# Kernel tuning notes

Hardware: AMD Instinct MI355X
Metric: run time of the kernel (lower is better)

Reference implementation:

```python
import jax, jax.numpy as jnp
import numpy as np

B, S, I, H, L = 32, 512, 512, 512, 2


def _gru_scan(x, wx, bx, wh, bh, reverse):
    # x: [B, S, layer_in_dim]; wx: [3H, in], wh: [3H, H]. PyTorch gate order r,z,n.
    hdim = wh.shape[1]
    gx = jnp.einsum('bsi,gi->sbg', x, wx) + bx  # precompute input gates: [S, B, 3H]
    h0 = jnp.zeros((x.shape[0], hdim), x.dtype)

    def step(h, gxt):
        gh = h @ wh.T + bh
        r = jax.nn.sigmoid(gxt[:, :hdim] + gh[:, :hdim])
        z = jax.nn.sigmoid(gxt[:, hdim:2 * hdim] + gh[:, hdim:2 * hdim])
        n = jnp.tanh(gxt[:, 2 * hdim:] + r * gh[:, 2 * hdim:])
        hn = (1 - z) * n + z * h
        return hn, hn

    hN, ys = jax.lax.scan(step, h0, gx, reverse=reverse)
    return ys.transpose(1, 0, 2), hN  # [B, S, H], [B, H]


def setup_inputs() -> dict:
    key = jax.random.key(0)
    ks = jax.random.split(key, 17)
    sc = 0.05
    d = {'x': jax.random.normal(ks[0], (B, S, I), jnp.float32)}
    i = 1
    for layer in range(L):
        in_dim = I if layer == 0 else 2 * H
        for tag in ('f', 'b'):
            d[f'wx_{tag}{layer}'] = jax.random.normal(ks[i], (3 * H, in_dim), jnp.float32) * sc
            d[f'bx_{tag}{layer}'] = jax.random.normal(jax.random.fold_in(ks[i], 1), (3 * H,), jnp.float32) * sc
            d[f'wh_{tag}{layer}'] = jax.random.normal(jax.random.fold_in(ks[i], 2), (3 * H, H), jnp.float32) * sc
            d[f'bh_{tag}{layer}'] = jax.random.normal(jax.random.fold_in(ks[i], 3), (3 * H,), jnp.float32) * sc
            i += 1
    return d


def reference(x,
              wx_f0, bx_f0, wh_f0, bh_f0, wx_b0, bx_b0, wh_b0, bh_b0,
              wx_f1, bx_f1, wh_f1, bh_f1, wx_b1, bx_b1, wh_b1, bh_b1):
    layers = [((wx_f0, bx_f0, wh_f0, bh_f0), (wx_b0, bx_b0, wh_b0, bh_b0)),
              ((wx_f1, bx_f1, wh_f1, bh_f1), (wx_b1, bx_b1, wh_b1, bh_b1))]
    layer_in = x
    h_fw, h_bw = [], []
    for fw, bw in layers:
        yf, hf = _gru_scan(layer_in, *fw, reverse=False)
        yb, hb = _gru_scan(layer_in, *bw, reverse=True)
        layer_in = jnp.concatenate([yf, yb], axis=-1)  # [B, S, 2H] (dropout p=0 -> identity)
        h_fw.append(hf)
        h_bw.append(hb)
    return layer_in, (jnp.stack(h_fw, 0), jnp.stack(h_bw, 0))
```

## Files before the change

kernel.cpp:

```cpp
#include <hip/hip_runtime.h>
#include <stdint.h>

typedef short short8 __attribute__((ext_vector_type(8)));
typedef float floatx4 __attribute__((ext_vector_type(4)));
typedef unsigned long long u64;

__device__ __forceinline__ unsigned short f2bf(float f) {
  union { float f; unsigned int i; } v;
  v.f = f;
  unsigned int r = v.i + 0x7fffu + ((v.i >> 16) & 1u);
  return (unsigned short)(r >> 16);
}
__device__ __forceinline__ short8 cvt8(const float4 a, const float4 b) {
  short8 v;
  v[0] = (short)f2bf(a.x); v[1] = (short)f2bf(a.y);
  v[2] = (short)f2bf(a.z); v[3] = (short)f2bf(a.w);
  v[4] = (short)f2bf(b.x); v[5] = (short)f2bf(b.y);
  v[6] = (short)f2bf(b.z); v[7] = (short)f2bf(b.w);
  return v;
}
__device__ __forceinline__ float sane(float x, float lim) {
  return fminf(fmaxf(x, -lim), lim);
}

extern __shared__ unsigned short lds[];

template<int K, int XM, int EM>
__global__ __launch_bounds__(128)
void gru_layer(const float* __restrict__ xf,
               const unsigned short* __restrict__ xb,
               const float* __restrict__ wxfp,
               const float* __restrict__ bxfp,
               const float* __restrict__ whfp,
               const float* __restrict__ bhfp,
               const float* __restrict__ wxbp,
               const float* __restrict__ bxbp,
               const float* __restrict__ whbp,
               const float* __restrict__ bhbp,
               unsigned short* __restrict__ exch,
               float* __restrict__ omain,
               float* __restrict__ out_hf,
               float* __restrict__ out_hb)
{
  constexpr int NKS = K / 32;
  constexpr int WXW = K + 8;
  constexpr int KC = K >> 3;
  constexpr int KSH = (K == 512) ? 6 : 7;
  constexpr u64 TM = 0x4000400040004000ULL;

  unsigned short* whs = lds;
  unsigned short* wxs = lds + 48 * 520;

  const int bid = blockIdx.x;
  const bool fw = bid < 32;
  const int d = fw ? bid : bid - 32;
  const int tid = threadIdx.x;
  const int lane = tid & 63;
  const int w = tid >> 6;
  const int q = lane >> 4;
  const int l16 = lane & 15;

  const float* wx = fw ? wxfp : wxbp;
  const float* bx = fw ? bxfp : bxbp;
  const float* wh = fw ? whfp : whbp;
  const float* bh = fw ? bhfp : bhbp;
  const int col0 = d * 16;
  const int dirofs = fw ? 0 : 512;

  unsigned int* exch32 = (unsigned int*)exch;

  for (int c = tid; c < 48 * 64; c += 128) {
    int lr = c >> 6, c8 = (c & 63) * 8;
    int g = lr >> 4, jc = lr & 15;
    const float* src = wh + (long)(g * 512 + col0 + jc) * 512 + c8;
    *(short8*)(whs + lr * 520 + c8) =
        cvt8(*(const float4*)src, *(const float4*)(src + 4));
  }
  for (int c = tid; c < 48 * KC; c += 128) {
    int lr = c >> KSH, c8 = (c & (KC - 1)) * 8;
    int g = lr >> 4, jc = lr & 15;
    const float* src = wx + (long)(g * 512 + col0 + jc) * K + c8;
    *(short8*)(wxs + lr * WXW + c8) =
        cvt8(*(const float4*)src, *(const float4*)(src + 4));
  }
  __syncthreads();

  const int jj = l16;
  const int gcr = col0 + jj;
  const int gcz = 512 + col0 + jj;
  const int gcn = 1024 + col0 + jj;
  const float cr = bx[gcr] + bh[gcr];
  const float cz = bx[gcz] + bh[gcz];
  const float bxn = bx[gcn];
  const float bhn = bh[gcn];

  const int cb = w * 16 + q * 4;
  const int ab = w * 16 + l16;

  const floatx4 fz = {0.f, 0.f, 0.f, 0.f};
  float h[4] = {0.f, 0.f, 0.f, 0.f};

  float4 fpre[XM ? 2 * NKS : 1];
  short8 bpre[XM ? 1 : NKS];

  auto load_x = [&](int t) {
    if (XM) {
      const float* p = xf + ((long)ab * 512 + t) * 512 + q * 8;
#pragma unroll
      for (int ks = 0; ks < NKS; ++ks) {
        fpre[2 * ks]     = *(const float4*)(p + ks * 32);
        fpre[2 * ks + 1] = *(const float4*)(p + ks * 32 + 4);
      }
    } else {
      const unsigned short* p = xb + ((long)t * 32 + ab) * 1024 + q * 8;
#pragma unroll
      for (int ks = 0; ks < NKS; ++ks)
        bpre[ks] = *(const short8*)(p + ks * 32);
    }
  };

  auto mfma_gx = [&](floatx4& gr, floatx4& gz, floatx4& gn) {
    gr = fz; gz = fz; gn = fz;
#pragma unroll
    for (int ks = 0; ks < NKS; ++ks) {
      short8 a;
      if (XM) {
        a = cvt8(fpre[2 * ks], fpre[2 * ks + 1]);
      } else {
        union { short8 s; unsigned int dd[4]; } u;
        u.s = bpre[ks];
        u.dd[0] &= 0xBFFFBFFFu; u.dd[1] &= 0xBFFFBFFFu;
        u.dd[2] &= 0xBFFFBFFFu; u.dd[3] &= 0xBFFFBFFFu;
        a = u.s;
      }
      short8 vr = *(const short8*)(wxs + (jj) * WXW + ks * 32 + q * 8);
      short8 vz = *(const short8*)(wxs + (16 + jj) * WXW + ks * 32 + q * 8);
      short8 vn = *(const short8*)(wxs + (32 + jj) * WXW + ks * 32 + q * 8);
      gr = __builtin_amdgcn_mfma_f32_16x16x32_bf16(a, vr, gr, 0, 0, 0);
      gz = __builtin_amdgcn_mfma_f32_16x16x32_bf16(a, vz, gz, 0, 0, 0);
      gn = __builtin_amdgcn_mfma_f32_16x16x32_bf16(a, vn, gn, 0, 0, 0);
    }
  };

  floatx4 gxr, gxz, gxn;
  { const int t0 = fw ? 0 : 511; load_x(t0); mfma_gx(gxr, gxz, gxn); }

  union W { u64 u[2]; short8 s; unsigned int dd[4]; };

  for (int it = 0; it < 512; ++it) {
    const int t = fw ? it : 511 - it;

    const unsigned short* hbase = nullptr;
    u64 expectw = 0;
    if (it > 0) {
      if (EM == 0) {
        const int tprev = fw ? t - 1 : t + 1;
        hbase = exch + ((long)tprev * 32 + ab) * 1024 + dirofs;
        expectw = TM;
      } else {
        const int slot_r = (it + 1) & 1;
        hbase = exch + ((long)slot_r * 32 + ab) * 1024 + dirofs;
        expectw = ((((it - 1) >> 1) & 1) ^ 1) ? TM : 0ULL;
      }
    }

    W wv[16];
    if (it > 0) {
#pragma unroll
      for (int ks = 0; ks < 16; ++ks) {
        u64* p = (u64*)(hbase + ks * 32 + q * 8);
        wv[ks].u[0] = __hip_atomic_load(p,     __ATOMIC_RELAXED, __HIP_MEMORY_SCOPE_AGENT);
        wv[ks].u[1] = __hip_atomic_load(p + 1, __ATOMIC_RELAXED, __HIP_MEMORY_SCOPE_AGENT);
      }
    }
    if (it < 511) {
      const int tn2 = fw ? (it + 1) : (511 - (it + 1));
      load_x(tn2);
    }

    floatx4 ar = fz, az = fz, an = fz;
    if (it > 0) {
      while (true) {
        u64 bad = 0;
#pragma unroll
        for (int ks = 0; ks < 16; ++ks)
          bad |= ((wv[ks].u[0] ^ expectw) | (wv[ks].u[1] ^ expectw)) & TM;
        if (bad == 0) break;
        __builtin_amdgcn_s_sleep(1);
#pragma unroll
        for (int ks = 0; ks < 16; ++ks) {
          u64* p = (u64*)(hbase + ks * 32 + q * 8);
          wv[ks].u[0] = __hip_atomic_load(p,     __ATOMIC_RELAXED, __HIP_MEMORY_SCOPE_AGENT);
          wv[ks].u[1] = __hip_atomic_load(p + 1, __ATOMIC_RELAXED, __HIP_MEMORY_SCOPE_AGENT);
        }
      }
#pragma unroll
      for (int ks = 0; ks < 16; ++ks) {
        wv[ks].dd[0] &= 0xBFFFBFFFu; wv[ks].dd[1] &= 0xBFFFBFFFu;
        wv[ks].dd[2] &= 0xBFFFBFFFu; wv[ks].dd[3] &= 0xBFFFBFFFu;
        short8 a = wv[ks].s;
        short8 vr = *(const short8*)(whs + (jj) * 520 + ks * 32 + q * 8);
        short8 vz = *(const short8*)(whs + (16 + jj) * 520 + ks * 32 + q * 8);
        short8 vn = *(const short8*)(whs + (32 + jj) * 520 + ks * 32 + q * 8);
        ar = __builtin_amdgcn_mfma_f32_16x16x32_bf16(a, vr, ar, 0, 0, 0);
        az = __builtin_amdgcn_mfma_f32_16x16x32_bf16(a, vz, az, 0, 0, 0);
        an = __builtin_amdgcn_mfma_f32_16x16x32_bf16(a, vn, an, 0, 0, 0);
      }
    }

    unsigned short hb16[4];
#pragma unroll
    for (int r = 0; r < 4; ++r) {
      const float xr = sane(gxr[r] + ar[r] + cr, 60.f);
      const float xz = sane(gxz[r] + az[r] + cz, 60.f);
      const float rr = 1.f / (1.f + __expf(-xr));
      const float zz = 1.f / (1.f + __expf(-xz));
      const float xn = sane(gxn[r] + bxn + rr * (an[r] + bhn), 30.f);
      const float e2 = __expf(-2.f * xn);
      const float nn = (1.f - e2) / (1.f + e2);
      h[r] = (1.f - zz) * nn + zz * h[r];
      hb16[r] = f2bf(h[r]);
    }

    const unsigned int tb =
        (EM == 0) ? 0x40004000u
                  : (((((it) >> 1) & 1) ^ 1) ? 0x40004000u : 0u);
    unsigned int hw[4];
#pragma unroll
    for (int r = 0; r < 4; ++r) {
      int v = hb16[r];
      int pmate = __shfl_xor(v, 1);
      hw[r] = ((unsigned int)(v & 0xffff) |
               ((unsigned int)(pmate & 0xffff) << 16)) | tb;
    }
    if ((jj & 1) == 0) {
      const int colw = (dirofs + col0 + jj) >> 1;
#pragma unroll
      for (int r = 0; r < 4; ++r) {
        const long eidx = (EM == 0)
            ? (((long)t * 32 + cb + r) * 512 + colw)
            : (((long)(it & 1) * 32 + cb + r) * 512 + colw);
        __hip_atomic_store(exch32 + eidx, hw[r],
                           __ATOMIC_RELAXED, __HIP_MEMORY_SCOPE_AGENT);
      }
    }
    if (EM == 1) {
#pragma unroll
      for (int r = 0; r < 4; ++r)
        omain[(long)(cb + r) * 524288 + (long)t * 1024 + dirofs + col0 + jj] = h[r];
    }

    if (it == 511) {
      float* oh = fw ? out_hf : out_hb;
#pragma unroll
      for (int r = 0; r < 4; ++r)
        oh[(cb + r) * 512 + col0 + jj] = h[r];
    } else {
      mfma_gx(gxr, gxz, gxn);
    }
  }
}

extern "C" void kernel_launch(void* const* d_in, const int* in_sizes, int n_in,
                              void* d_out, int out_size, void* d_ws, size_t ws_size,
                              hipStream_t stream)
{
  (void)in_sizes; (void)n_in; (void)out_size; (void)ws_size;

  const float* x    = (const float*)d_in[0];
  const float* wxf0 = (const float*)d_in[1];
  const float* bxf0 = (const float*)d_in[2];
  const float* whf0 = (const float*)d_in[3];
  const float* bhf0 = (const float*)d_in[4];
  const float* wxb0 = (const float*)d_in[5];
  const float* bxb0 = (const float*)d_in[6];
  const float* whb0 = (const float*)d_in[7];
  const float* bhb0 = (const float*)d_in[8];
  const float* wxf1 = (const float*)d_in[9];
  const float* bxf1 = (const float*)d_in[10];
  const float* whf1 = (const float*)d_in[11];
  const float* bhf1 = (const float*)d_in[12];
  const float* wxb1 = (const float*)d_in[13];
  const float* bxb1 = (const float*)d_in[14];
  const float* whb1 = (const float*)d_in[15];
  const float* bhb1 = (const float*)d_in[16];

  char* ws = (char*)d_ws;
  unsigned short* y0    = (unsigned short*)(ws);
  unsigned short* ring1 = (unsigned short*)(ws + 33554432L);

  float* out = (float*)d_out;
  float* out_hf0 = out + 16777216L;
  float* out_hf1 = out + 16777216L + 16384L;
  float* out_hb0 = out + 16777216L + 32768L;
  float* out_hb1 = out + 16777216L + 49152L;

  const size_t lds0 = (size_t)(48 * 520 + 48 * (512 + 8)) * 2;
  const size_t lds1 = (size_t)(48 * 520 + 48 * (1024 + 8)) * 2;
  (void)hipFuncSetAttribute((const void*)gru_layer<512, 1, 0>,
                            hipFuncAttributeMaxDynamicSharedMemorySize, (int)lds0);
  (void)hipFuncSetAttribute((const void*)gru_layer<1024, 0, 1>,
                            hipFuncAttributeMaxDynamicSharedMemorySize, (int)lds1);

  hipMemsetAsync(ws, 0, 33685504L, stream);

  gru_layer<512, 1, 0><<<dim3(64), dim3(128), lds0, stream>>>(
      x, nullptr, wxf0, bxf0, whf0, bhf0, wxb0, bxb0, whb0, bhb0,
      y0, nullptr, out_hf0, out_hb0);

  gru_layer<1024, 0, 1><<<dim3(64), dim3(128), lds1, stream>>>(
      nullptr, y0, wxf1, bxf1, whf1, bhf1, wxb1, bxb1, whb1, bhb1,
      ring1, out, out_hf1, out_hb1);
}
```

Measured before the change: 6.993 ms.

## Hoist input-gate projection into batched GEMM and halve recurrent block count

Takes the per-timestep input-gate MFMA computation out of the sequential recurrence and runs it as a separate large bf16 MFMA GEMM per layer that writes fp32 gate pre-activations to workspace. The recurrent kernel then only prefetches those precomputed values and does the hidden-state matmul. It uses 32 blocks with 32 columns each instead of 64 blocks with 16, so fewer blocks take part in the cross-block spin-wait exchange. In exchange it adds a large fp32 gx write and read to global memory and gives each recurrent block twice the per-step hidden-matmul work.

```diff
diff --git a/kernel.cpp b/kernel.cpp
--- a/kernel.cpp
+++ b/kernel.cpp
@@ -25,143 +25,179 @@
 
 extern __shared__ unsigned short lds[];
 
-template<int K, int XM, int EM>
+template<int K, int XM>
+__global__ __launch_bounds__(256)
+void gx_gemm(const float* __restrict__ xf,
+             const unsigned short* __restrict__ xb,
+             const float* __restrict__ wxf,
+             const float* __restrict__ wxb,
+             float* __restrict__ gx)
+{
+  unsigned short* As = lds;
+  unsigned short* Bs = lds + 128 * 40;
+
+  const int M0 = blockIdx.x * 128;
+  const int N0 = blockIdx.y * 128;
+  const int dir = blockIdx.z;
+  const float* wx = dir ? wxb : wxf;
+  float* gxd = gx + (long)dir * 16384 * 1536;
+
+  const int tid = threadIdx.x;
+  const int lane = tid & 63;
+  const int wid = tid >> 6;
+  const int q = lane >> 4;
+  const int l16 = lane & 15;
+  const int wM = (wid >> 1) * 64;
+  const int wN = (wid & 1) * 64;
+
+  const int srow = tid >> 1;
+  const int k0 = (tid & 1) * 16;
+
+  floatx4 acc[4][4];
+#pragma unroll
+  for (int i = 0; i < 4; ++i)
+#pragma unroll
+    for (int j = 0; j < 4; ++j) acc[i][j] = (floatx4){0.f, 0.f, 0.f, 0.f};
+
+  for (int kk = 0; kk < K; kk += 32) {
+    __syncthreads();
+    {
+      const int mg = M0 + srow;
+      if (XM) {
+        const float* ap = xf + ((long)(mg & 31) * 512 + (mg >> 5)) * 512 + kk + k0;
+        float4 f0 = *(const float4*)(ap);
+        float4 f1 = *(const float4*)(ap + 4);
+        float4 f2 = *(const float4*)(ap + 8);
+        float4 f3 = *(const float4*)(ap + 12);
+        *(short8*)(As + srow * 40 + k0)     = cvt8(f0, f1);
+        *(short8*)(As + srow * 40 + k0 + 8) = cvt8(f2, f3);
+      } else {
+        const unsigned short* ap = xb + (long)mg * 1024 + kk + k0;
+        *(short8*)(As + srow * 40 + k0)     = *(const short8*)(ap);
+        *(short8*)(As + srow * 40 + k0 + 8) = *(const short8*)(ap + 8);
+      }
+      const float* bp = wx + (long)(N0 + srow) * K + kk + k0;
+      float4 g0 = *(const float4*)(bp);
+      float4 g1 = *(const float4*)(bp + 4);
+      float4 g2 = *(const float4*)(bp + 8);
+      float4 g3 = *(const float4*)(bp + 12);
+      *(short8*)(Bs + srow * 40 + k0)     = cvt8(g0, g1);
+      *(short8*)(Bs + srow * 40 + k0 + 8) = cvt8(g2, g3);
+    }
+    __syncthreads();
+    short8 a[4], b[4];
+#pragma unroll
+    for (int mt = 0; mt < 4; ++mt)
+      a[mt] = *(const short8*)(As + (wM + mt * 16 + l16) * 40 + q * 8);
+#pragma unroll
+    for (int nt = 0; nt < 4; ++nt)
+      b[nt] = *(const short8*)(Bs + (wN + nt * 16 + l16) * 40 + q * 8);
+#pragma unroll
+    for (int mt = 0; mt < 4; ++mt)
+#pragma unroll
+      for (int nt = 0; nt < 4; ++nt)
+        acc[mt][nt] = __builtin_amdgcn_mfma_f32_16x16x32_bf16(
+            a[mt], b[nt], acc[mt][nt], 0, 0, 0);
+  }
+#pragma unroll
+  for (int mt = 0; mt < 4; ++mt) {
+    const int row = M0 + wM + mt * 16 + q * 4;
+#pragma unroll
+    for (int nt = 0; nt < 4; ++nt) {
+      const int col = N0 + wN + nt * 16 + l16;
+#pragma unroll
+      for (int r = 0; r < 4; ++r)
+        gxd[(long)(row + r) * 1536 + col] = acc[mt][nt][r];
+    }
+  }
+}
+
+template<int OUT>
 __global__ __launch_bounds__(128)
-void gru_layer(const float* __restrict__ xf,
-               const unsigned short* __restrict__ xb,
-               const float* __restrict__ wxfp,
-               const float* __restrict__ bxfp,
-               const float* __restrict__ whfp,
-               const float* __restrict__ bhfp,
-               const float* __restrict__ wxbp,
-               const float* __restrict__ bxbp,
-               const float* __restrict__ whbp,
-               const float* __restrict__ bhbp,
-               unsigned short* __restrict__ exch,
-               float* __restrict__ omain,
-               float* __restrict__ out_hf,
-               float* __restrict__ out_hb)
+void gru_rec(const float* __restrict__ gx,
+             const float* __restrict__ whfp, const float* __restrict__ bhfp,
+             const float* __restrict__ whbp, const float* __restrict__ bhbp,
+             const float* __restrict__ bxfp, const float* __restrict__ bxbp,
+             unsigned short* __restrict__ ring,
+             unsigned short* __restrict__ y0,
+             float* __restrict__ omain,
+             float* __restrict__ out_hf,
+             float* __restrict__ out_hb)
 {
-  constexpr int NKS = K / 32;
-  constexpr int WXW = K + 8;
-  constexpr int KC = K >> 3;
-  constexpr int KSH = (K == 512) ? 6 : 7;
   constexpr u64 TM = 0x4000400040004000ULL;
-
   unsigned short* whs = lds;
-  unsigned short* wxs = lds + 48 * 520;
 
   const int bid = blockIdx.x;
-  const bool fw = bid < 32;
-  const int d = fw ? bid : bid - 32;
+  const bool fw = bid < 16;
+  const int d = fw ? bid : bid - 16;
   const int tid = threadIdx.x;
   const int lane = tid & 63;
   const int w = tid >> 6;
   const int q = lane >> 4;
   const int l16 = lane & 15;
 
-  const float* wx = fw ? wxfp : wxbp;
-  const float* bx = fw ? bxfp : bxbp;
   const float* wh = fw ? whfp : whbp;
   const float* bh = fw ? bhfp : bhbp;
-  const int col0 = d * 16;
+  const float* bx = fw ? bxfp : bxbp;
+  const int col0 = d * 32;
   const int dirofs = fw ? 0 : 512;
-
-  unsigned int* exch32 = (unsigned int*)exch;
-
-  for (int c = tid; c < 48 * 64; c += 128) {
+  const float* gxd = gx + (long)(fw ? 0 : 1) * 16384 * 1536;
+
+  for (int c = tid; c < 96 * 64; c += 128) {
     int lr = c >> 6, c8 = (c & 63) * 8;
-    int g = lr >> 4, jc = lr & 15;
+    int g = lr >> 5, jc = lr & 31;
     const float* src = wh + (long)(g * 512 + col0 + jc) * 512 + c8;
     *(short8*)(whs + lr * 520 + c8) =
         cvt8(*(const float4*)src, *(const float4*)(src + 4));
   }
-  for (int c = tid; c < 48 * KC; c += 128) {
-    int lr = c >> KSH, c8 = (c & (KC - 1)) * 8;
-    int g = lr >> 4, jc = lr & 15;
-    const float* src = wx + (long)(g * 512 + col0 + jc) * K + c8;
-    *(short8*)(wxs + lr * WXW + c8) =
-        cvt8(*(const float4*)src, *(const float4*)(src + 4));
-  }
   __syncthreads();
 
   const int jj = l16;
-  const int gcr = col0 + jj;
-  const int gcz = 512 + col0 + jj;
-  const int gcn = 1024 + col0 + jj;
-  const float cr = bx[gcr] + bh[gcr];
-  const float cz = bx[gcz] + bh[gcz];
-  const float bxn = bx[gcn];
-  const float bhn = bh[gcn];
+  float cr[2], cz[2], bxn[2], bhn[2];
+#pragma unroll
+  for (int n2 = 0; n2 < 2; ++n2) {
+    const int cc = col0 + n2 * 16 + jj;
+    cr[n2] = bx[cc] + bh[cc];
+    cz[n2] = bx[512 + cc] + bh[512 + cc];
+    bxn[n2] = bx[1024 + cc];
+    bhn[n2] = bh[1024 + cc];
+  }
 
   const int cb = w * 16 + q * 4;
   const int ab = w * 16 + l16;
-
   const floatx4 fz = {0.f, 0.f, 0.f, 0.f};
-  float h[4] = {0.f, 0.f, 0.f, 0.f};
-
-  float4 fpre[XM ? 2 * NKS : 1];
-  short8 bpre[XM ? 1 : NKS];
-
-  auto load_x = [&](int t) {
-    if (XM) {
-      const float* p = xf + ((long)ab * 512 + t) * 512 + q * 8;
-#pragma unroll
-      for (int ks = 0; ks < NKS; ++ks) {
-        fpre[2 * ks]     = *(const float4*)(p + ks * 32);
-        fpre[2 * ks + 1] = *(const float4*)(p + ks * 32 + 4);
-      }
-    } else {
-      const unsigned short* p = xb + ((long)t * 32 + ab) * 1024 + q * 8;
-#pragma unroll
-      for (int ks = 0; ks < NKS; ++ks)
-        bpre[ks] = *(const short8*)(p + ks * 32);
-    }
+  float h[2][4] = {{0.f, 0.f, 0.f, 0.f}, {0.f, 0.f, 0.f, 0.f}};
+  unsigned int* ring32 = (unsigned int*)ring;
+  unsigned int* y032 = (unsigned int*)y0;
+
+  float nx[24];
+  auto load_gx = [&](int t) {
+    const float* base = gxd + (long)t * 32 * 1536;
+#pragma unroll
+    for (int g = 0; g < 3; ++g)
+#pragma unroll
+      for (int n2 = 0; n2 < 2; ++n2)
+#pragma unroll
+        for (int r = 0; r < 4; ++r)
+          nx[(g * 2 + n2) * 4 + r] =
+              base[(long)(cb + r) * 1536 + g * 512 + col0 + n2 * 16 + jj];
   };
-
-  auto mfma_gx = [&](floatx4& gr, floatx4& gz, floatx4& gn) {
-    gr = fz; gz = fz; gn = fz;
-#pragma unroll
-    for (int ks = 0; ks < NKS; ++ks) {
-      short8 a;
-      if (XM) {
-        a = cvt8(fpre[2 * ks], fpre[2 * ks + 1]);
-      } else {
-        union { short8 s; unsigned int dd[4]; } u;
-        u.s = bpre[ks];
-        u.dd[0] &= 0xBFFFBFFFu; u.dd[1] &= 0xBFFFBFFFu;
-        u.dd[2] &= 0xBFFFBFFFu; u.dd[3] &= 0xBFFFBFFFu;
-        a = u.s;
-      }
-      short8 vr = *(const short8*)(wxs + (jj) * WXW + ks * 32 + q * 8);
-      short8 vz = *(const short8*)(wxs + (16 + jj) * WXW + ks * 32 + q * 8);
-      short8 vn = *(const short8*)(wxs + (32 + jj) * WXW + ks * 32 + q * 8);
-      gr = __builtin_amdgcn_mfma_f32_16x16x32_bf16(a, vr, gr, 0, 0, 0);
-      gz = __builtin_amdgcn_mfma_f32_16x16x32_bf16(a, vz, gz, 0, 0, 0);
-      gn = __builtin_amdgcn_mfma_f32_16x16x32_bf16(a, vn, gn, 0, 0, 0);
-    }
-  };
-
-  floatx4 gxr, gxz, gxn;
-  { const int t0 = fw ? 0 : 511; load_x(t0); mfma_gx(gxr, gxz, gxn); }
+  { const int t0 = fw ? 0 : 511; load_gx(t0); }
 
   union W { u64 u[2]; short8 s; unsigned int dd[4]; };
 
   for (int it = 0; it < 512; ++it) {
     const int t = fw ? it : 511 - it;
+    float cur[24];
+#pragma unroll
+    for (int i = 0; i < 24; ++i) cur[i] = nx[i];
 
     const unsigned short* hbase = nullptr;
     u64 expectw = 0;
     if (it > 0) {
-      if (EM == 0) {
-        const int tprev = fw ? t - 1 : t + 1;
-        hbase = exch + ((long)tprev * 32 + ab) * 1024 + dirofs;
-        expectw = TM;
-      } else {
-        const int slot_r = (it + 1) & 1;
-        hbase = exch + ((long)slot_r * 32 + ab) * 1024 + dirofs;
-        expectw = ((((it - 1) >> 1) & 1) ^ 1) ? TM : 0ULL;
-      }
+      const int slot_r = (it + 1) & 1;
+      hbase = ring + ((long)slot_r * 32 + ab) * 1024 + dirofs;
+      expectw = ((((it - 1) >> 1) & 1) ^ 1) ? TM : 0ULL;
     }
 
     W wv[16];
@@ -174,11 +210,11 @@
       }
     }
     if (it < 511) {
-      const int tn2 = fw ? (it + 1) : (511 - (it + 1));
-      load_x(tn2);
-    }
-
-    floatx4 ar = fz, az = fz, an = fz;
+      const int tn = fw ? it + 1 : 511 - (it + 1);
+      load_gx(tn);
+    }
+
+    floatx4 ar[2] = {fz, fz}, az[2] = {fz, fz}, an[2] = {fz, fz};
     if (it > 0) {
       while (true) {
         u64 bad = 0;
@@ -199,64 +235,70 @@
         wv[ks].dd[0] &= 0xBFFFBFFFu; wv[ks].dd[1] &= 0xBFFFBFFFu;
         wv[ks].dd[2] &= 0xBFFFBFFFu; wv[ks].dd[3] &= 0xBFFFBFFFu;
         short8 a = wv[ks].s;
-        short8 vr = *(const short8*)(whs + (jj) * 520 + ks * 32 + q * 8);
-        short8 vz = *(const short8*)(whs + (16 + jj) * 520 + ks * 32 + q * 8);
-        short8 vn = *(const short8*)(whs + (32 + jj) * 520 + ks * 32 + q * 8);
-        ar = __builtin_amdgcn_mfma_f32_16x16x32_bf16(a, vr, ar, 0, 0, 0);
-        az = __builtin_amdgcn_mfma_f32_16x16x32_bf16(a, vz, az, 0, 0, 0);
-        an = __builtin_amdgcn_mfma_f32_16x16x32_bf16(a, vn, an, 0, 0, 0);
-      }
-    }
-
-    unsigned short hb16[4];
-#pragma unroll
-    for (int r = 0; r < 4; ++r) {
-      const float xr = sane(gxr[r] + ar[r] + cr, 60.f);
-      const float xz = sane(gxz[r] + az[r] + cz, 60.f);
-      const float rr = 1.f / (1.f + __expf(-xr));
-      const float zz = 1.f / (1.f + __expf(-xz));
-      const float xn = sane(gxn[r] + bxn + rr * (an[r] + bhn), 30.f);
-      const float e2 = __expf(-2.f * xn);
-      const float nn = (1.f - e2) / (1.f + e2);
-      h[r] = (1.f - zz) * nn + zz * h[r];
-      hb16[r] = f2bf(h[r]);
-    }
-
-    const unsigned int tb =
-        (EM == 0) ? 0x40004000u
-                  : (((((it) >> 1) & 1) ^ 1) ? 0x40004000u : 0u);
-    unsigned int hw[4];
-#pragma unroll
-    for (int r = 0; r < 4; ++r) {
-      int v = hb16[r];
-      int pmate = __shfl_xor(v, 1);
-      hw[r] = ((unsigned int)(v & 0xffff) |
-               ((unsigned int)(pmate & 0xffff) << 16)) | tb;
-    }
+#pragma unroll
+        for (int n2 = 0; n2 < 2; ++n2) {
+          short8 vr = *(const short8*)(whs + (n2 * 16 + jj) * 520 + ks * 32 + q * 8);
+          short8 vz = *(const short8*)(whs + (32 + n2 * 16 + jj) * 520 + ks * 32 + q * 8);
+          short8 vn = *(const short8*)(whs + (64 + n2 * 16 + jj) * 520 + ks * 32 + q * 8);
+          ar[n2] = __builtin_amdgcn_mfma_f32_16x16x32_bf16(a, vr, ar[n2], 0, 0, 0);
+          az[n2] = __builtin_amdgcn_mfma_f32_16x16x32_bf16(a, vz, az[n2], 0, 0, 0);
+          an[n2] = __builtin_amdgcn_mfma_f32_16x16x32_bf16(a, vn, an[n2], 0, 0, 0);
+        }
+      }
+    }
+
+    unsigned int hwp[2][4];
+#pragma unroll
+    for (int n2 = 0; n2 < 2; ++n2) {
+#pragma unroll
+      for (int r = 0; r < 4; ++r) {
+        const float xr = sane(cur[(0 * 2 + n2) * 4 + r] + ar[n2][r] + cr[n2], 60.f);
+        const float xz = sane(cur[(1 * 2 + n2) * 4 + r] + az[n2][r] + cz[n2], 60.f);
+        const float rr = 1.f / (1.f + __expf(-xr));
+        const float zz = 1.f / (1.f + __expf(-xz));
+        const float xn = sane(cur[(2 * 2 + n2) * 4 + r] + bxn[n2] +
+                              rr * (an[n2][r] + bhn[n2]), 30.f);
+        const float e2 = __expf(-2.f * xn);
+        const float nn = (1.f - e2) / (1.f + e2);
+        h[n2][r] = (1.f - zz) * nn + zz * h[n2][r];
+        int v = f2bf(h[n2][r]);
+        int pm = __shfl_xor(v, 1);
+        hwp[n2][r] = (unsigned int)(v & 0xffff) |
+                     ((unsigned int)(pm & 0xffff) << 16);
+      }
+    }
+
+    const unsigned int tb = (((it >> 1) & 1) ^ 1) ? 0x40004000u : 0u;
+    const int slot_w = it & 1;
     if ((jj & 1) == 0) {
-      const int colw = (dirofs + col0 + jj) >> 1;
-#pragma unroll
-      for (int r = 0; r < 4; ++r) {
-        const long eidx = (EM == 0)
-            ? (((long)t * 32 + cb + r) * 512 + colw)
-            : (((long)(it & 1) * 32 + cb + r) * 512 + colw);
-        __hip_atomic_store(exch32 + eidx, hw[r],
-                           __ATOMIC_RELAXED, __HIP_MEMORY_SCOPE_AGENT);
-      }
-    }
-    if (EM == 1) {
-#pragma unroll
-      for (int r = 0; r < 4; ++r)
-        omain[(long)(cb + r) * 524288 + (long)t * 1024 + dirofs + col0 + jj] = h[r];
-    }
-
+#pragma unroll
+      for (int n2 = 0; n2 < 2; ++n2) {
+        const int colw = (dirofs + col0 + n2 * 16 + jj) >> 1;
+#pragma unroll
+        for (int r = 0; r < 4; ++r) {
+          __hip_atomic_store(ring32 + ((long)slot_w * 32 + cb + r) * 512 + colw,
+                             hwp[n2][r] | tb,
+                             __ATOMIC_RELAXED, __HIP_MEMORY_SCOPE_AGENT);
+          if (OUT == 0)
+            y032[((long)t * 32 + cb + r) * 512 + colw] = hwp[n2][r];
+        }
+      }
+    }
+    if (OUT == 1) {
+#pragma unroll
+      for (int n2 = 0; n2 < 2; ++n2)
+#pragma unroll
+        for (int r = 0; r < 4; ++r)
+          omain[(long)(cb + r) * 524288 + (long)t * 1024 +
+                dirofs + col0 + n2 * 16 + jj] = h[n2][r];
+    }
     if (it == 511) {
       float* oh = fw ? out_hf : out_hb;
 #pragma unroll
-      for (int r = 0; r < 4; ++r)
-        oh[(cb + r) * 512 + col0 + jj] = h[r];
-    } else {
-      mfma_gx(gxr, gxz, gxn);
+      for (int n2 = 0; n2 < 2; ++n2)
+#pragma unroll
+        for (int r = 0; r < 4; ++r)
+          oh[(cb + r) * 512 + col0 + n2 * 16 + jj] = h[n2][r];
     }
   }
 }
@@ -286,8 +328,10 @@
   const float* bhb1 = (const float*)d_in[16];
 
   char* ws = (char*)d_ws;
-  unsigned short* y0    = (unsigned short*)(ws);
-  unsigned short* ring1 = (unsigned short*)(ws + 33554432L);
+  float* gx             = (float*)(ws);
+  unsigned short* y0    = (unsigned short*)(ws + 201326592L);
+  unsigned short* ring0 = (unsigned short*)(ws + 234881024L);
+  unsigned short* ring1 = (unsigned short*)(ws + 235012096L);
 
   float* out = (float*)d_out;
   float* out_hf0 = out + 16777216L;
@@ -295,20 +339,23 @@
   float* out_hb0 = out + 16777216L + 32768L;
   float* out_hb1 = out + 16777216L + 49152L;
 
-  const size_t lds0 = (size_t)(48 * 520 + 48 * (512 + 8)) * 2;
-  const size_t lds1 = (size_t)(48 * 520 + 48 * (1024 + 8)) * 2;
-  (void)hipFuncSetAttribute((const void*)gru_layer<512, 1, 0>,
-                            hipFuncAttributeMaxDynamicSharedMemorySize, (int)lds0);
-  (void)hipFuncSetAttribute((const void*)gru_layer<1024, 0, 1>,
-                            hipFuncAttributeMaxDynamicSharedMemorySize, (int)lds1);
-
-  hipMemsetAsync(ws, 0, 33685504L, stream);
-
-  gru_layer<512, 1, 0><<<dim3(64), dim3(128), lds0, stream>>>(
-      x, nullptr, wxf0, bxf0, whf0, bhf0, wxb0, bxb0, whb0, bhb0,
-      y0, nullptr, out_hf0, out_hb0);
-
-  gru_layer<1024, 0, 1><<<dim3(64), dim3(128), lds1, stream>>>(
-      nullptr, y0, wxf1, bxf1, whf1, bhf1, wxb1, bxb1, whb1, bhb1,
-      ring1, out, out_hf1, out_hb1);
-}
+  const size_t lds_gemm = (size_t)(2 * 128 * 40) * 2;
+  const size_t lds_rec  = (size_t)(96 * 520) * 2;
+  (void)hipFuncSetAttribute((const void*)gru_rec<0>,
+                            hipFuncAttributeMaxDynamicSharedMemorySize, (int)lds_rec);
+  (void)hipFuncSetAttribute((const void*)gru_rec<1>,
+                            hipFuncAttributeMaxDynamicSharedMemorySize, (int)lds_rec);
+
+  hipMemsetAsync(ws + 234881024L, 0, 262144L, stream);
+
+  gx_gemm<512, 1><<<dim3(128, 12, 2), dim3(256), lds_gemm, stream>>>(
+      x, nullptr, wxf0, wxb0, gx);
+  gru_rec<0><<<dim3(32), dim3(128), lds_rec, stream>>>(
+      gx, whf0, bhf0, whb0, bhb0, bxf0, bxb0,
+      ring0, y0, nullptr, out_hf0, out_hb0);
+  gx_gemm<1024, 0><<<dim3(128, 12, 2), dim3(256), lds_gemm, stream>>>(
+      nullptr, y0, wxf1, wxb1, gx);
+  gru_rec<1><<<dim3(32), dim3(128), lds_rec, stream>>>(
+      gx, whf1, bhf1, whb1, bhb1, bxf1, bxb1,
+      ring1, nullptr, out, out_hf1, out_hb1);
+}
```

After: 7.077 ms. No clear change (+1.2%).
